# Kernel optimization log

Measured on AMD Instinct MI355X. Metric: run time of the kernel, lower is better.

The kernel has to match this reference:

```python
import jax, jax.numpy as jnp
import numpy as np


def _binarize_act(z):
    # STE: forward = sign(z), backward = d/dz clamp(z,-1,1)
    clipped = jnp.clip(z, -1.0, 1.0)
    return jax.lax.stop_gradient(jnp.sign(z) - clipped) + clipped


def _binarize_weight(w):
    # per-output-channel scaling factor = mean |w| over (in, kh, kw), detached
    scale = jax.lax.stop_gradient(jnp.mean(jnp.abs(w), axis=(1, 2, 3), keepdims=True))
    clipped = jnp.clip(w, -1.0, 1.0)
    return jax.lax.stop_gradient(scale * jnp.sign(w) - clipped) + clipped


def setup_inputs() -> dict:
    key = jax.random.key(0)
    k = jax.random.split(key, 6)
    B, C, H, W = 16, 64, 256, 256
    return {
        "x": jax.random.normal(k[0], (B, C, H, W), dtype=jnp.float32),
        "move0_bias": jax.random.normal(k[1], (1, C, 1, 1), dtype=jnp.float32) * 0.1,
        "conv_weight": jax.random.normal(k[2], (C, C, 3, 3), dtype=jnp.float32) * 0.1,
        "prelu_weight": jnp.full((C,), 0.25, dtype=jnp.float32)
        + jax.random.normal(k[3], (C,), dtype=jnp.float32) * 0.01,
        "pr_bias0": jax.random.normal(k[4], (1, C, 1, 1), dtype=jnp.float32) * 0.1,
        "pr_bias1": jax.random.normal(k[5], (1, C, 1, 1), dtype=jnp.float32) * 0.1,
    }


def reference(x, move0_bias, conv_weight, prelu_weight, pr_bias0, pr_bias1):
    identity = x  # stride=1, out_channels == in_channels -> no downsample / concat
    z = _binarize_act(x + move0_bias)
    bw = _binarize_weight(conv_weight)
    y = jax.lax.conv_general_dilated(
        z, bw, window_strides=(1, 1), padding=((1, 1), (1, 1)),
        dimension_numbers=("NCHW", "OIHW", "NCHW"))
    # RPReLU: bias0 -> per-channel PReLU -> bias1
    y = y + pr_bias0
    a = prelu_weight.reshape(1, -1, 1, 1)
    y = jnp.where(y > 0, y, a * y)
    y = y + pr_bias1
    return y + identity
```

## Files before the change

### kernel.cpp

```cpp
#include <hip/hip_runtime.h>
#include <stdint.h>

#define Bn 16
#define C 64
#define H 256
#define W 256
#define HW (H * W)
#define NHW (Bn * HW)

__global__ void prep_weights(const float* __restrict__ w,
                             uint64_t* __restrict__ wbits,
                             float* __restrict__ scale) {
    int o = blockIdx.x;
    int c = threadIdx.x;
    const float* wp = w + ((size_t)o * C + c) * 9;
    float asum = 0.f;
#pragma unroll
    for (int tap = 0; tap < 9; ++tap) {
        float v = wp[tap];
        asum += fabsf(v);
        uint64_t m = __ballot(v > 0.f);
        if (c == 0) wbits[o * 9 + tap] = m;
    }
#pragma unroll
    for (int off = 32; off > 0; off >>= 1)
        asum += __shfl_down(asum, off);
    if (c == 0) scale[o] = asum * (1.f / 576.f);
}

__global__ __launch_bounds__(256) void pack_z(const float* __restrict__ x,
                                              const float* __restrict__ bias,
                                              uint64_t* __restrict__ zbits) {
    int p = blockIdx.x * 256 + threadIdx.x;
    int n = p >> 16;
    int hw = p & (HW - 1);
    const float* xp = x + (size_t)n * C * HW + hw;
    uint64_t bits = 0;
#pragma unroll
    for (int c = 0; c < C; ++c) {
        float v = xp[(size_t)c * HW] + bias[c];
        bits |= (uint64_t)(v > 0.f) << c;
    }
    zbits[p] = bits;
}

__global__ __launch_bounds__(256) void bconv(const uint64_t* __restrict__ zbits,
                                             const uint64_t* __restrict__ wbits,
                                             const float* __restrict__ scale,
                                             const float* __restrict__ x,
                                             const float* __restrict__ pb0,
                                             const float* __restrict__ aw,
                                             const float* __restrict__ pb1,
                                             float* __restrict__ out) {
    __shared__ uint64_t swb[576];
    __shared__ float sscale[C], spb0[C], sa[C], spb1[C];
    int t = threadIdx.x;
    if (t < C) {
        sscale[t] = scale[t];
        spb0[t]   = pb0[t];
        sa[t]     = aw[t];
        spb1[t]   = pb1[t];
    }
    for (int i = t; i < 576; i += 256) swb[i] = wbits[i];
    __syncthreads();

    int p = blockIdx.x * 256 + t;
    int n = p >> 16;
    int hw = p & (HW - 1);
    int h = hw >> 8;
    int w = hw & (W - 1);

    const uint64_t* zrow = zbits + (size_t)n * HW;
    uint64_t zb[9];
    int vmask[9];
    int nvalid = 0;
#pragma unroll
    for (int dh = -1; dh <= 1; ++dh) {
#pragma unroll
        for (int dw = -1; dw <= 1; ++dw) {
            int tap = (dh + 1) * 3 + (dw + 1);
            int hh = h + dh, ww = w + dw;
            bool valid = ((unsigned)hh < (unsigned)H) && ((unsigned)ww < (unsigned)W);
            vmask[tap] = valid ? -1 : 0;
            nvalid += valid ? 1 : 0;
            zb[tap] = valid ? zrow[hh * W + ww] : 0ull;
        }
    }

    const float* xid = x + (size_t)n * C * HW + hw;
    float* op = out + (size_t)n * C * HW + hw;
    int base = 64 * nvalid;

#pragma unroll 4
    for (int o = 0; o < C; ++o) {
        const uint64_t* wp = &swb[o * 9];
        int s = 0;
#pragma unroll
        for (int tap = 0; tap < 9; ++tap)
            s += vmask[tap] & (int)__popcll(wp[tap] ^ zb[tap]);
        float y = sscale[o] * (float)(base - 2 * s) + spb0[o];
        y = y > 0.f ? y : sa[o] * y;
        y += spb1[o];
        op[(size_t)o * HW] = y + xid[(size_t)o * HW];
    }
}

extern "C" void kernel_launch(void* const* d_in, const int* in_sizes, int n_in,
                              void* d_out, int out_size, void* d_ws, size_t ws_size,
                              hipStream_t stream) {
    const float* x           = (const float*)d_in[0];
    const float* move0_bias  = (const float*)d_in[1];
    const float* conv_weight = (const float*)d_in[2];
    const float* prelu_w     = (const float*)d_in[3];
    const float* pr_bias0    = (const float*)d_in[4];
    const float* pr_bias1    = (const float*)d_in[5];
    float* out = (float*)d_out;

    uint8_t* ws = (uint8_t*)d_ws;
    uint64_t* zbits = (uint64_t*)ws;
    uint64_t* wbits = (uint64_t*)(ws + (size_t)NHW * 8);
    float* scale    = (float*)(ws + (size_t)NHW * 8 + 576 * 8);

    prep_weights<<<64, 64, 0, stream>>>(conv_weight, wbits, scale);
    pack_z<<<NHW / 256, 256, 0, stream>>>(x, move0_bias, zbits);
    bconv<<<NHW / 256, 256, 0, stream>>>(zbits, wbits, scale, x,
                                         pr_bias0, prelu_w, pr_bias1, out);
}
```

Baseline: 548.4 us.

## Process four pixels per thread with float4 I/O and sliding bit window

Both the packing and binary-conv kernels now handle four adjacent pixels per thread using float4 loads and stores. The conv kernel loads a 3x6 window of packed activation bits once and reuses it across the four outputs. It also reads weight bits directly from global memory instead of staging them in LDS, and packs the per-channel epilogue parameters into one float4. The aim is to cut per-element memory instructions and redundant neighbour loads, at the cost of more registers and a quarter as many threads.

Measured after the change: 556.0 us. Within noise of the previous version (+1.4%).

```diff
diff --git a/kernel.cpp b/kernel.cpp
--- a/kernel.cpp
+++ b/kernel.cpp
@@ -6,11 +6,15 @@
 #define H 256
 #define W 256
 #define HW (H * W)
+#define HW4 (HW / 4)
 #define NHW (Bn * HW)
 
 __global__ void prep_weights(const float* __restrict__ w,
+                             const float* __restrict__ pb0,
+                             const float* __restrict__ aw,
+                             const float* __restrict__ pb1,
                              uint64_t* __restrict__ wbits,
-                             float* __restrict__ scale) {
+                             float4* __restrict__ params) {
     int o = blockIdx.x;
     int c = threadIdx.x;
     const float* wp = w + ((size_t)o * C + c) * 9;
@@ -25,83 +29,131 @@
 #pragma unroll
     for (int off = 32; off > 0; off >>= 1)
         asum += __shfl_down(asum, off);
-    if (c == 0) scale[o] = asum * (1.f / 576.f);
+    if (c == 0)
+        params[o] = make_float4(asum * (1.f / 576.f), pb0[o], aw[o], pb1[o]);
 }
 
-__global__ __launch_bounds__(256) void pack_z(const float* __restrict__ x,
-                                              const float* __restrict__ bias,
-                                              uint64_t* __restrict__ zbits) {
+__global__ __launch_bounds__(256) void pack_z4(const float* __restrict__ x,
+                                               const float* __restrict__ bias,
+                                               uint64_t* __restrict__ zbits) {
     int p = blockIdx.x * 256 + threadIdx.x;
-    int n = p >> 16;
-    int hw = p & (HW - 1);
-    const float* xp = x + (size_t)n * C * HW + hw;
-    uint64_t bits = 0;
-#pragma unroll
+    int n = p >> 14;
+    int hw4 = (p & (HW4 - 1)) << 2;
+    const float* xp = x + ((size_t)n << 22) + hw4;
+    uint64_t b0 = 0, b1 = 0, b2 = 0, b3 = 0;
+#pragma unroll 8
     for (int c = 0; c < C; ++c) {
-        float v = xp[(size_t)c * HW] + bias[c];
-        bits |= (uint64_t)(v > 0.f) << c;
+        float4 v = *(const float4*)(xp + ((size_t)c << 16));
+        float bc = bias[c];
+        b0 |= (uint64_t)(v.x + bc > 0.f) << c;
+        b1 |= (uint64_t)(v.y + bc > 0.f) << c;
+        b2 |= (uint64_t)(v.z + bc > 0.f) << c;
+        b3 |= (uint64_t)(v.w + bc > 0.f) << c;
     }
-    zbits[p] = bits;
+    uint64_t* zp = zbits + ((size_t)n << 16) + hw4;
+    uint4 lo = make_uint4((uint32_t)b0, (uint32_t)(b0 >> 32),
+                          (uint32_t)b1, (uint32_t)(b1 >> 32));
+    uint4 hi = make_uint4((uint32_t)b2, (uint32_t)(b2 >> 32),
+                          (uint32_t)b3, (uint32_t)(b3 >> 32));
+    *(uint4*)zp = lo;
+    *((uint4*)zp + 1) = hi;
 }
 
-__global__ __launch_bounds__(256) void bconv(const uint64_t* __restrict__ zbits,
-                                             const uint64_t* __restrict__ wbits,
-                                             const float* __restrict__ scale,
-                                             const float* __restrict__ x,
-                                             const float* __restrict__ pb0,
-                                             const float* __restrict__ aw,
-                                             const float* __restrict__ pb1,
-                                             float* __restrict__ out) {
-    __shared__ uint64_t swb[576];
-    __shared__ float sscale[C], spb0[C], sa[C], spb1[C];
-    int t = threadIdx.x;
-    if (t < C) {
-        sscale[t] = scale[t];
-        spb0[t]   = pb0[t];
-        sa[t]     = aw[t];
-        spb1[t]   = pb1[t];
-    }
-    for (int i = t; i < 576; i += 256) swb[i] = wbits[i];
-    __syncthreads();
+__global__ __launch_bounds__(256) void bconv4(const uint64_t* __restrict__ zbits,
+                                              const uint64_t* __restrict__ wbits,
+                                              const float4* __restrict__ params,
+                                              const float* __restrict__ x,
+                                              float* __restrict__ out) {
+    int p = blockIdx.x * 256 + threadIdx.x;
+    int n = p >> 14;
+    int hw4 = (p & (HW4 - 1)) << 2;
+    int h = hw4 >> 8;
+    int w0 = hw4 & (W - 1);
 
-    int p = blockIdx.x * 256 + t;
-    int n = p >> 16;
-    int hw = p & (HW - 1);
-    int h = hw >> 8;
-    int w = hw & (W - 1);
+    const uint64_t* zimg = zbits + ((size_t)n << 16);
 
-    const uint64_t* zrow = zbits + (size_t)n * HW;
-    uint64_t zb[9];
-    int vmask[9];
-    int nvalid = 0;
+    uint64_t zwin[3][6];
+    int rm[3], rmc0[3], rmc5[3];
+    int cm0 = (w0 > 0) ? -1 : 0;
+    int cm5 = (w0 < W - 4) ? -1 : 0;
+    int c0 = (w0 > 0) ? w0 - 1 : 0;
 #pragma unroll
-    for (int dh = -1; dh <= 1; ++dh) {
-#pragma unroll
-        for (int dw = -1; dw <= 1; ++dw) {
-            int tap = (dh + 1) * 3 + (dw + 1);
-            int hh = h + dh, ww = w + dw;
-            bool valid = ((unsigned)hh < (unsigned)H) && ((unsigned)ww < (unsigned)W);
-            vmask[tap] = valid ? -1 : 0;
-            nvalid += valid ? 1 : 0;
-            zb[tap] = valid ? zrow[hh * W + ww] : 0ull;
-        }
+    for (int r = 0; r < 3; ++r) {
+        int hh = h - 1 + r;
+        bool rv = (unsigned)hh < (unsigned)H;
+        rm[r] = rv ? -1 : 0;
+        rmc0[r] = rm[r] & cm0;
+        rmc5[r] = rm[r] & cm5;
+        int hc = rv ? hh : h;
+        const uint64_t* zr = zimg + hc * W;
+        zwin[r][0] = zr[c0];
+        zwin[r][1] = zr[w0];
+        zwin[r][2] = zr[w0 + 1];
+        zwin[r][3] = zr[w0 + 2];
+        zwin[r][4] = zr[w0 + 3];
+        zwin[r][5] = zr[w0 + 4];
     }
 
-    const float* xid = x + (size_t)n * C * HW + hw;
-    float* op = out + (size_t)n * C * HW + hw;
-    int base = 64 * nvalid;
+    int base[4];
+#pragma unroll
+    for (int j = 0; j < 4; ++j) {
+        int nv = 0;
+#pragma unroll
+        for (int r = 0; r < 3; ++r)
+#pragma unroll
+            for (int cc = 0; cc < 3; ++cc) {
+                int k = j + cc;
+                int mk = (k == 0) ? rmc0[r] : (k == 5) ? rmc5[r] : rm[r];
+                nv += mk & 1;
+            }
+        base[j] = nv << 6;
+    }
 
-#pragma unroll 4
+    const float* xbase = x + ((size_t)n << 22) + hw4;
+    float* obase = out + ((size_t)n << 22) + hw4;
+
     for (int o = 0; o < C; ++o) {
-        const uint64_t* wp = &swb[o * 9];
-        int s = 0;
+        const uint64_t* wp = wbits + o * 9;
+        uint64_t wv[9];
 #pragma unroll
-        for (int tap = 0; tap < 9; ++tap)
-            s += vmask[tap] & (int)__popcll(wp[tap] ^ zb[tap]);
-        float y = sscale[o] * (float)(base - 2 * s) + spb0[o];
-        y = y > 0.f ? y : sa[o] * y;
-        y += spb1[o];
-        op[(size_t)o * HW] = y + xid[(size_t)o * HW];
+        for (int t9 = 0; t9 < 9; ++t9) wv[t9] = wp[t9];
+
+        int s0 = 0, s1 = 0, s2 = 0, s3 = 0;
+#pragma unroll
+        for (int r = 0; r < 3; ++r) {
+#pragma unroll
+            for (int cc = 0; cc < 3; ++cc) {
+                uint64_t wt = wv[r * 3 + cc];
+                {
+                    int mk = (cc == 0) ? rmc0[r] : rm[r];
+                    s0 += mk & (int)__popcll(wt ^ zwin[r][cc]);
+                }
+                {
+                    s1 += rm[r] & (int)__popcll(wt ^ zwin[r][1 + cc]);
+                }
+                {
+                    s2 += rm[r] & (int)__popcll(wt ^ zwin[r][2 + cc]);
+                }
+                {
+                    int mk = (cc == 2) ? rmc5[r] : rm[r];
+                    s3 += mk & (int)__popcll(wt ^ zwin[r][3 + cc]);
+                }
+            }
+        }
+
+        float4 pr = params[o];
+        float4 xi = *(const float4*)(xbase + ((size_t)o << 16));
+
+        float y0 = pr.x * (float)(base[0] - 2 * s0) + pr.y;
+        float y1 = pr.x * (float)(base[1] - 2 * s1) + pr.y;
+        float y2 = pr.x * (float)(base[2] - 2 * s2) + pr.y;
+        float y3 = pr.x * (float)(base[3] - 2 * s3) + pr.y;
+        y0 = (y0 > 0.f ? y0 : pr.z * y0) + pr.w + xi.x;
+        y1 = (y1 > 0.f ? y1 : pr.z * y1) + pr.w + xi.y;
+        y2 = (y2 > 0.f ? y2 : pr.z * y2) + pr.w + xi.z;
+        y3 = (y3 > 0.f ? y3 : pr.z * y3) + pr.w + xi.w;
+
+        *(float4*)(obase + ((size_t)o << 16)) = make_float4(y0, y1, y2, y3);
     }
 }
 
@@ -119,10 +171,10 @@
     uint8_t* ws = (uint8_t*)d_ws;
     uint64_t* zbits = (uint64_t*)ws;
     uint64_t* wbits = (uint64_t*)(ws + (size_t)NHW * 8);
-    float* scale    = (float*)(ws + (size_t)NHW * 8 + 576 * 8);
+    float4* params  = (float4*)(ws + (size_t)NHW * 8 + 640 * 8);
 
-    prep_weights<<<64, 64, 0, stream>>>(conv_weight, wbits, scale);
-    pack_z<<<NHW / 256, 256, 0, stream>>>(x, move0_bias, zbits);
-    bconv<<<NHW / 256, 256, 0, stream>>>(zbits, wbits, scale, x,
-                                         pr_bias0, prelu_w, pr_bias1, out);
+    prep_weights<<<64, 64, 0, stream>>>(conv_weight, pr_bias0, prelu_w,
+                                        pr_bias1, wbits, params);
+    pack_z4<<<NHW / 1024, 256, 0, stream>>>(x, move0_bias, zbits);
+    bconv4<<<NHW / 1024, 256, 0, stream>>>(zbits, wbits, params, x, out);
 }
```
